# Kernel optimization log

Hardware: AMD Instinct MI355X
Metric: run time of the kernel (lower is better)

## Reference

```python
import jax, jax.numpy as jnp
import numpy as np

B, SQ, SKV, D = 16, 2048, 2048, 256

def setup_inputs() -> dict:
    key = jax.random.key(0)
    k1, k2, k3 = jax.random.split(key, 3)
    x = jax.random.normal(k1, (B, SQ, D), dtype=jnp.float32)
    y = jax.random.normal(k2, (B, SKV, D), dtype=jnp.float32)
    attn_mask = jax.random.normal(k3, (B, SQ, SKV), dtype=jnp.float32)
    dropout = 0  # p=0 -> deterministic (F.dropout with p=0 is identity)
    return {"x": x, "y": y, "attn_mask": attn_mask, "dropout": dropout}

def reference(x, y, attn_mask, dropout):
    # qk = x @ y^T : [B, Sq, Skv]
    qk = jnp.einsum('bqd,bkd->bqk', x, y)
    # NOTE: original scales mask by 1/sqrt(y.size(-2)) = 1/sqrt(Skv), not sqrt(D)
    scale_factor = attn_mask / (y.shape[-2] ** 0.5)
    scaled_qk = qk * scale_factor  # multiplicative per-element mask
    softmax_qk = jax.nn.softmax(scaled_qk, axis=-1)
    # dropout p=0 -> identity (deterministic baseline)
    dropout_qk = softmax_qk
    output = jnp.einsum('bqk,bkd->bqd', dropout_qk, y)
    return output + x
```

## Files before the change

kernel.cpp:

```cpp
#include <hip/hip_runtime.h>
#include <stdint.h>

typedef unsigned short u16;
typedef unsigned int   u32;

#define NB   16
#define SQL  2048
#define SKVL 2048
#define DHD  256
#define BQ   64
#define BKV  32
#define NITER (SKVL / BKV)
#define KSS  264
#define VTG  328
#define PSS  40
#define SCALE 0.022097086912079612f

typedef __bf16 bf16x8 __attribute__((ext_vector_type(8)));
typedef float  f32x4  __attribute__((ext_vector_type(4)));

__device__ __forceinline__ u16 f2b(float f) {
    union { float f; u32 i; } v; v.f = f;
    u32 x = v.i;
    return (u16)((x + 0x7fffu + ((x >> 16) & 1u)) >> 16);
}

__global__ __launch_bounds__(256, 2)
void fa_kernel(const float* __restrict__ x, const float* __restrict__ y,
               const float* __restrict__ mask, float* __restrict__ out)
{
    __shared__ __align__(16) u16 Ks[BKV * KSS];
    __shared__ __align__(16) u32 Vt[16 * VTG];
    __shared__ __align__(16) u16 Ps[BQ * PSS];

    const int tid  = threadIdx.x;
    const int wv   = tid >> 6;
    const int lane = tid & 63;
    const int l16  = lane & 15;
    const int quad = lane >> 4;

    const int b  = blockIdx.x >> 5;
    const int q0 = (blockIdx.x & 31) * BQ;

    bf16x8 qfrag[8];
    {
        const float* xq = x + ((size_t)(b * SQL + q0 + wv * 16 + l16)) * DHD + quad * 8;
        #pragma unroll
        for (int s = 0; s < 8; ++s) {
            const float4 a = *(const float4*)(xq + s * 32);
            const float4 c = *(const float4*)(xq + s * 32 + 4);
            union { u32 w[4]; bf16x8 v; } u;
            u.w[0] = (u32)f2b(a.x) | ((u32)f2b(a.y) << 16);
            u.w[1] = (u32)f2b(a.z) | ((u32)f2b(a.w) << 16);
            u.w[2] = (u32)f2b(c.x) | ((u32)f2b(c.y) << 16);
            u.w[3] = (u32)f2b(c.z) | ((u32)f2b(c.w) << 16);
            qfrag[s] = u.v;
        }
    }

    f32x4 o[16] = {};
    float lsum[4] = {0.f, 0.f, 0.f, 0.f};

    const int kv2 = tid & 15;
    const int dc  = tid >> 4;
    const float* ybase = y + ((size_t)b * SKVL) * DHD;

    float4 r0[4], r1[4];
    {
        const float* p0 = ybase + (size_t)(2 * kv2) * DHD + dc * 16;
        const float* p1 = p0 + DHD;
        #pragma unroll
        for (int p = 0; p < 4; ++p) { r0[p] = *(const float4*)(p0 + p * 4);
                                      r1[p] = *(const float4*)(p1 + p * 4); }
    }

    const float* mbase = mask + ((size_t)(b * SQL + q0 + wv * 16 + quad * 4)) * SKVL;

    float mkc0[4], mkc1[4], mkn0[4], mkn1[4];
    #pragma unroll
    for (int r = 0; r < 4; ++r) {
        const float* mp = mbase + (size_t)r * SKVL;
        mkc0[r] = mp[l16];
        mkc1[r] = mp[16 + l16];
    }

    for (int it = 0; it < NITER; ++it) {
        const int kv0 = it * BKV;

        __syncthreads();
        {
            u16 e0[16], e1[16];
            #pragma unroll
            for (int p = 0; p < 4; ++p) {
                e0[p*4+0]=f2b(r0[p].x); e0[p*4+1]=f2b(r0[p].y);
                e0[p*4+2]=f2b(r0[p].z); e0[p*4+3]=f2b(r0[p].w);
                e1[p*4+0]=f2b(r1[p].x); e1[p*4+1]=f2b(r1[p].y);
                e1[p*4+2]=f2b(r1[p].z); e1[p*4+3]=f2b(r1[p].w);
            }
            union { u32 w[4]; uint4 q; } k0a, k0b, k1a, k1b;
            #pragma unroll
            for (int i = 0; i < 4; ++i) {
                k0a.w[i] = (u32)e0[2*i]     | ((u32)e0[2*i+1]   << 16);
                k0b.w[i] = (u32)e0[8+2*i]   | ((u32)e0[8+2*i+1] << 16);
                k1a.w[i] = (u32)e1[2*i]     | ((u32)e1[2*i+1]   << 16);
                k1b.w[i] = (u32)e1[8+2*i]   | ((u32)e1[8+2*i+1] << 16);
            }
            *(uint4*)(&Ks[(2*kv2)  *KSS + dc*16])     = k0a.q;
            *(uint4*)(&Ks[(2*kv2)  *KSS + dc*16 + 8]) = k0b.q;
            *(uint4*)(&Ks[(2*kv2+1)*KSS + dc*16])     = k1a.q;
            *(uint4*)(&Ks[(2*kv2+1)*KSS + dc*16 + 8]) = k1b.q;
            #pragma unroll
            for (int e = 0; e < 16; ++e)
                Vt[dc*VTG + e*20 + kv2] = (u32)e0[e] | ((u32)e1[e] << 16);
        }
        __syncthreads();

        if (it + 1 < NITER) {
            const float* p0 = ybase + (size_t)(kv0 + BKV + 2 * kv2) * DHD + dc * 16;
            const float* p1 = p0 + DHD;
            #pragma unroll
            for (int p = 0; p < 4; ++p) { r0[p] = *(const float4*)(p0 + p * 4);
                                          r1[p] = *(const float4*)(p1 + p * 4); }
        }

        {
            const int kvn = (it + 1 < NITER) ? (kv0 + BKV) : 0;
            #pragma unroll
            for (int r = 0; r < 4; ++r) {
                const float* mp = mbase + (size_t)r * SKVL + kvn;
                mkn0[r] = mp[l16];
                mkn1[r] = mp[16 + l16];
            }
        }

        f32x4 acc0 = {}, acc1 = {};
        #pragma unroll
        for (int s = 0; s < 8; ++s) {
            bf16x8 b0 = *(const bf16x8*)(&Ks[ l16      * KSS + s*32 + quad*8]);
            bf16x8 b1 = *(const bf16x8*)(&Ks[(16+l16)  * KSS + s*32 + quad*8]);
            acc0 = __builtin_amdgcn_mfma_f32_16x16x32_bf16(qfrag[s], b0, acc0, 0, 0, 0);
            acc1 = __builtin_amdgcn_mfma_f32_16x16x32_bf16(qfrag[s], b1, acc1, 0, 0, 0);
        }

        #pragma unroll
        for (int r = 0; r < 4; ++r) {
            float p0 = __expf(acc0[r] * mkc0[r] * SCALE);
            float p1 = __expf(acc1[r] * mkc1[r] * SCALE);
            lsum[r] += p0 + p1;
            u16* pr = &Ps[(wv*16 + quad*4 + r) * PSS];
            pr[l16]      = f2b(p0);
            pr[16 + l16] = f2b(p1);
        }

        bf16x8 afrag = *(const bf16x8*)(&Ps[(wv*16 + l16) * PSS + quad*8]);
        #pragma unroll
        for (int t = 0; t < 16; ++t) {
            bf16x8 bfrag = *(const bf16x8*)(&Vt[t*VTG + l16*20 + quad*4]);
            o[t] = __builtin_amdgcn_mfma_f32_16x16x32_bf16(afrag, bfrag, o[t], 0, 0, 0);
        }

        #pragma unroll
        for (int r = 0; r < 4; ++r) { mkc0[r] = mkn0[r]; mkc1[r] = mkn1[r]; }
    }

    #pragma unroll
    for (int r = 0; r < 4; ++r) {
        float v = lsum[r];
        v += __shfl_xor(v, 1);
        v += __shfl_xor(v, 2);
        v += __shfl_xor(v, 4);
        v += __shfl_xor(v, 8);
        lsum[r] = 1.0f / v;
    }

    const int qrow = q0 + wv * 16 + quad * 4;
    #pragma unroll
    for (int r = 0; r < 4; ++r) {
        const size_t rowoff = ((size_t)(b * SQL + qrow + r)) * DHD;
        #pragma unroll
        for (int t = 0; t < 16; ++t) {
            const int d = t * 16 + l16;
            out[rowoff + d] = o[t][r] * lsum[r] + x[rowoff + d];
        }
    }
}

extern "C" void kernel_launch(void* const* d_in, const int* in_sizes, int n_in,
                              void* d_out, int out_size, void* d_ws, size_t ws_size,
                              hipStream_t stream) {
    const float* x    = (const float*)d_in[0];
    const float* y    = (const float*)d_in[1];
    const float* mask = (const float*)d_in[2];
    float* out        = (float*)d_out;
    dim3 grid(NB * (SQL / BQ));
    fa_kernel<<<grid, 256, 0, stream>>>(x, y, mask, out);
}
```

Measured before the change: 501.7 us.

## Precompute bf16 K and transposed V in workspace, stream via async LDS loads

Adds a prepass kernel that converts y to bf16 once, in both a row-major swizzled layout for K and a transposed swizzled layout for V, and stores them in the workspace. The main kernel then uses direct global-to-LDS async copies of these tiles with 64-wide KV blocks and 32x32x16 MFMAs. Waves are split across query and KV halves, and row sums are reduced through shared memory. This removes the per-block fp32-to-bf16 conversion and scattered transposition of y, in exchange for an extra kernel launch, workspace traffic and more barriers per iteration. A fallback keeps the old kernel when the workspace is too small.

```diff
diff --git a/kernel.cpp b/kernel.cpp
--- a/kernel.cpp
+++ b/kernel.cpp
@@ -8,16 +8,11 @@
 #define SQL  2048
 #define SKVL 2048
 #define DHD  256
-#define BQ   64
-#define BKV  32
-#define NITER (SKVL / BKV)
-#define KSS  264
-#define VTG  328
-#define PSS  40
 #define SCALE 0.022097086912079612f
 
 typedef __bf16 bf16x8 __attribute__((ext_vector_type(8)));
 typedef float  f32x4  __attribute__((ext_vector_type(4)));
+typedef float  f32x16 __attribute__((ext_vector_type(16)));
 
 __device__ __forceinline__ u16 f2b(float f) {
     union { float f; u32 i; } v; v.f = f;
@@ -25,22 +20,243 @@
     return (u16)((x + 0x7fffu + ((x >> 16) & 1u)) >> 16);
 }
 
+__device__ __forceinline__ void async_cp16(const void* g, void* l) {
+    __builtin_amdgcn_global_load_lds(
+        (const __attribute__((address_space(1))) u32*)g,
+        (__attribute__((address_space(3))) u32*)l, 16, 0, 0);
+}
+
+__global__ __launch_bounds__(256)
+void prepass(const float* __restrict__ y, u16* __restrict__ ws)
+{
+    u16* yb  = ws;
+    u16* ybT = ws + 8388608;
+
+    const int tid = threadIdx.x;
+    if (blockIdx.x < 512) {
+        const int b   = blockIdx.x >> 5;
+        const int seg = blockIdx.x & 31;
+        const int r   = tid >> 2;
+        const int dq  = tid & 3;
+        const int kvg = seg * 64 + r;
+        const float* src = y + ((size_t)(b * SKVL + kvg)) * DHD + dq * 64;
+        u16* dst = yb + ((size_t)(b * SKVL + kvg)) * DHD;
+        #pragma unroll
+        for (int j = 0; j < 8; ++j) {
+            const float4 a = *(const float4*)(src + j * 8);
+            const float4 c4 = *(const float4*)(src + j * 8 + 4);
+            union { u32 w[4]; uint4 q; } u;
+            u.w[0] = (u32)f2b(a.x)  | ((u32)f2b(a.y)  << 16);
+            u.w[1] = (u32)f2b(a.z)  | ((u32)f2b(a.w)  << 16);
+            u.w[2] = (u32)f2b(c4.x) | ((u32)f2b(c4.y) << 16);
+            u.w[3] = (u32)f2b(c4.z) | ((u32)f2b(c4.w) << 16);
+            const int pos = (dq * 8 + j) ^ (kvg & 7);
+            *(uint4*)(dst + pos * 8) = u.q;
+        }
+    } else {
+        const int j     = blockIdx.x - 512;
+        const int b     = j >> 5;
+        const int kvblk = j & 31;
+        const int d     = tid;
+        const int kv0   = kvblk * 64;
+        u16* dst = ybT + ((size_t)(b * 32 + kvblk)) * 16384 + d * 64;
+        #pragma unroll
+        for (int c = 0; c < 8; ++c) {
+            float v[8];
+            #pragma unroll
+            for (int e = 0; e < 8; ++e)
+                v[e] = y[((size_t)(b * SKVL + kv0 + 8 * c + e)) * DHD + d];
+            union { u32 w[4]; uint4 q; } u;
+            #pragma unroll
+            for (int i = 0; i < 4; ++i)
+                u.w[i] = (u32)f2b(v[2 * i]) | ((u32)f2b(v[2 * i + 1]) << 16);
+            const int p = c ^ (d & 7);
+            *(uint4*)(dst + p * 8) = u.q;
+        }
+    }
+}
+
 __global__ __launch_bounds__(256, 2)
-void fa_kernel(const float* __restrict__ x, const float* __restrict__ y,
-               const float* __restrict__ mask, float* __restrict__ out)
+void fa_main(const float* __restrict__ x, const float* __restrict__ mask,
+             const u16* __restrict__ ws, float* __restrict__ out)
 {
-    __shared__ __align__(16) u16 Ks[BKV * KSS];
-    __shared__ __align__(16) u32 Vt[16 * VTG];
-    __shared__ __align__(16) u16 Ps[BQ * PSS];
+    __shared__ __align__(16) u16 Ks[16384];
+    __shared__ __align__(16) u16 Vt[16384];
+    __shared__ __align__(16) u16 Ps[64 * 72];
+    __shared__ float Lred[2][64];
+
+    const u16* yb  = ws;
+    const u16* ybT = ws + 8388608;
+
+    const int tid  = threadIdx.x;
+    const int wv   = tid >> 6;
+    const int lane = tid & 63;
+    const int n    = lane & 31;
+    const int hi   = lane >> 5;
+    const int qh   = wv & 1;
+    const int kh   = wv >> 1;
+
+    const int b  = blockIdx.x >> 5;
+    const int q0 = (blockIdx.x & 31) * 64;
+
+    bf16x8 qfrag[16];
+    {
+        const float* xq = x + ((size_t)(b * SQL + q0 + 32 * qh + n)) * DHD + 8 * hi;
+        #pragma unroll
+        for (int s = 0; s < 16; ++s) {
+            const float4 a  = *(const float4*)(xq + s * 16);
+            const float4 c4 = *(const float4*)(xq + s * 16 + 4);
+            union { u32 w[4]; bf16x8 v; } u;
+            u.w[0] = (u32)f2b(a.x)  | ((u32)f2b(a.y)  << 16);
+            u.w[1] = (u32)f2b(a.z)  | ((u32)f2b(a.w)  << 16);
+            u.w[2] = (u32)f2b(c4.x) | ((u32)f2b(c4.y) << 16);
+            u.w[3] = (u32)f2b(c4.z) | ((u32)f2b(c4.w) << 16);
+            qfrag[s] = u.v;
+        }
+    }
+
+    f32x16 o0 = {}, o1 = {}, o2 = {}, o3 = {};
+    float lsum[16];
+    #pragma unroll
+    for (int r = 0; r < 16; ++r) lsum[r] = 0.f;
+
+    const float* mrow = mask + ((size_t)(b * SQL + q0 + 32 * qh + 4 * hi)) * SKVL
+                             + 32 * kh + n;
+    #define ROFF(r) ((size_t)(((r) & 3) + 8 * ((r) >> 2)) * SKVL)
+
+    float mkc[16], mkn[16];
+    #pragma unroll
+    for (int r = 0; r < 16; ++r) mkc[r] = mrow[ROFF(r)];
+
+    {
+        const char* gk = (const char*)(yb + ((size_t)b * SKVL) * DHD) + wv * 8192 + lane * 16;
+        const char* gv = (const char*)(ybT + ((size_t)b * 32) * 16384) + wv * 8192 + lane * 16;
+        char* lk = ((char*)Ks) + wv * 8192;
+        char* lv = ((char*)Vt) + wv * 8192;
+        #pragma unroll
+        for (int i = 0; i < 8; ++i) { async_cp16(gk + i * 1024, lk + i * 1024);
+                                      async_cp16(gv + i * 1024, lv + i * 1024); }
+    }
+    __syncthreads();
+
+    for (int it = 0; it < 32; ++it) {
+        const size_t kvn = (it + 1 < 32) ? (size_t)(it + 1) * 64 : 0;
+        #pragma unroll
+        for (int r = 0; r < 16; ++r) mkn[r] = mrow[ROFF(r) + kvn];
+
+        f32x16 sacc = {};
+        const int kvloc = 32 * kh + n;
+        #pragma unroll
+        for (int s = 0; s < 16; ++s) {
+            const int p = (2 * s + hi) ^ (kvloc & 7);
+            bf16x8 bf = *(const bf16x8*)(&Ks[kvloc * 256 + p * 8]);
+            sacc = __builtin_amdgcn_mfma_f32_32x32x16_bf16(qfrag[s], bf, sacc, 0, 0, 0);
+        }
+
+        #pragma unroll
+        for (int r = 0; r < 16; ++r) {
+            const int rowloc = (r & 3) + 8 * (r >> 2) + 4 * hi;
+            float pv = __expf(sacc[r] * mkc[r] * SCALE);
+            lsum[r] += pv;
+            Ps[(32 * qh + rowloc) * 72 + 32 * kh + n] = f2b(pv);
+        }
+
+        __syncthreads();
+
+        if (it + 1 < 32) {
+            const char* gk = (const char*)(yb + ((size_t)(b * SKVL + (it + 1) * 64)) * DHD)
+                             + wv * 8192 + lane * 16;
+            char* lk = ((char*)Ks) + wv * 8192;
+            #pragma unroll
+            for (int i = 0; i < 8; ++i) async_cp16(gk + i * 1024, lk + i * 1024);
+        }
+
+        bf16x8 pa[4];
+        #pragma unroll
+        for (int s = 0; s < 4; ++s)
+            pa[s] = *(const bf16x8*)(&Ps[(32 * qh + n) * 72 + 16 * s + 8 * hi]);
+        #pragma unroll
+        for (int t = 0; t < 4; ++t) {
+            const int d = 128 * kh + 32 * t + n;
+            f32x16 acc = (t == 0) ? o0 : (t == 1) ? o1 : (t == 2) ? o2 : o3;
+            #pragma unroll
+            for (int s = 0; s < 4; ++s) {
+                const int p = (2 * s + hi) ^ (d & 7);
+                bf16x8 bf = *(const bf16x8*)(&Vt[d * 64 + p * 8]);
+                acc = __builtin_amdgcn_mfma_f32_32x32x16_bf16(pa[s], bf, acc, 0, 0, 0);
+            }
+            if (t == 0) o0 = acc; else if (t == 1) o1 = acc; else if (t == 2) o2 = acc; else o3 = acc;
+        }
+
+        __syncthreads();
+
+        if (it + 1 < 32) {
+            const char* gv = (const char*)(ybT + ((size_t)(b * 32 + it + 1)) * 16384)
+                             + wv * 8192 + lane * 16;
+            char* lv = ((char*)Vt) + wv * 8192;
+            #pragma unroll
+            for (int i = 0; i < 8; ++i) async_cp16(gv + i * 1024, lv + i * 1024);
+        }
+        __syncthreads();
+
+        #pragma unroll
+        for (int r = 0; r < 16; ++r) mkc[r] = mkn[r];
+    }
+
+    #pragma unroll
+    for (int r = 0; r < 16; ++r) {
+        float v = lsum[r];
+        v += __shfl_xor(v, 1);
+        v += __shfl_xor(v, 2);
+        v += __shfl_xor(v, 4);
+        v += __shfl_xor(v, 8);
+        v += __shfl_xor(v, 16);
+        if (n == 0) {
+            const int rowloc = (r & 3) + 8 * (r >> 2) + 4 * hi;
+            Lred[kh][32 * qh + rowloc] = v;
+        }
+    }
+    __syncthreads();
+
+    float inv[16];
+    #pragma unroll
+    for (int r = 0; r < 16; ++r) {
+        const int qloc = 32 * qh + (r & 3) + 8 * (r >> 2) + 4 * hi;
+        inv[r] = 1.0f / (Lred[0][qloc] + Lred[1][qloc]);
+    }
+
+    #pragma unroll
+    for (int r = 0; r < 16; ++r) {
+        const int qloc = 32 * qh + (r & 3) + 8 * (r >> 2) + 4 * hi;
+        const size_t rowoff = ((size_t)(b * SQL + q0 + qloc)) * DHD;
+        #pragma unroll
+        for (int t = 0; t < 4; ++t) {
+            const int d = 128 * kh + 32 * t + n;
+            const float ov = (t == 0) ? o0[r] : (t == 1) ? o1[r] : (t == 2) ? o2[r] : o3[r];
+            out[rowoff + d] = ov * inv[r] + x[rowoff + d];
+        }
+    }
+}
+
+#define FKSS 264
+#define FVTG 328
+#define FPSS 40
+
+__global__ __launch_bounds__(256, 2)
+void fa_fallback(const float* __restrict__ x, const float* __restrict__ y,
+                 const float* __restrict__ mask, float* __restrict__ out)
+{
+    __shared__ __align__(16) u16 Ks[32 * FKSS];
+    __shared__ __align__(16) u32 Vt[16 * FVTG];
+    __shared__ __align__(16) u16 Ps[64 * FPSS];
 
     const int tid  = threadIdx.x;
     const int wv   = tid >> 6;
     const int lane = tid & 63;
     const int l16  = lane & 15;
     const int quad = lane >> 4;
-
     const int b  = blockIdx.x >> 5;
-    const int q0 = (blockIdx.x & 31) * BQ;
+    const int q0 = (blockIdx.x & 31) * 64;
 
     bf16x8 qfrag[8];
     {
@@ -57,14 +273,11 @@
             qfrag[s] = u.v;
         }
     }
-
     f32x4 o[16] = {};
-    float lsum[4] = {0.f, 0.f, 0.f, 0.f};
-
+    float ls[4] = {0.f, 0.f, 0.f, 0.f};
     const int kv2 = tid & 15;
     const int dc  = tid >> 4;
     const float* ybase = y + ((size_t)b * SKVL) * DHD;
-
     float4 r0[4], r1[4];
     {
         const float* p0 = ybase + (size_t)(2 * kv2) * DHD + dc * 16;
@@ -73,20 +286,15 @@
         for (int p = 0; p < 4; ++p) { r0[p] = *(const float4*)(p0 + p * 4);
                                       r1[p] = *(const float4*)(p1 + p * 4); }
     }
-
     const float* mbase = mask + ((size_t)(b * SQL + q0 + wv * 16 + quad * 4)) * SKVL;
-
     float mkc0[4], mkc1[4], mkn0[4], mkn1[4];
     #pragma unroll
     for (int r = 0; r < 4; ++r) {
         const float* mp = mbase + (size_t)r * SKVL;
-        mkc0[r] = mp[l16];
-        mkc1[r] = mp[16 + l16];
-    }
-
-    for (int it = 0; it < NITER; ++it) {
-        const int kv0 = it * BKV;
-
+        mkc0[r] = mp[l16]; mkc1[r] = mp[16 + l16];
+    }
+    for (int it = 0; it < 64; ++it) {
+        const int kv0 = it * 32;
         __syncthreads();
         {
             u16 e0[16], e1[16];
@@ -100,79 +308,68 @@
             union { u32 w[4]; uint4 q; } k0a, k0b, k1a, k1b;
             #pragma unroll
             for (int i = 0; i < 4; ++i) {
-                k0a.w[i] = (u32)e0[2*i]     | ((u32)e0[2*i+1]   << 16);
-                k0b.w[i] = (u32)e0[8+2*i]   | ((u32)e0[8+2*i+1] << 16);
-                k1a.w[i] = (u32)e1[2*i]     | ((u32)e1[2*i+1]   << 16);
-                k1b.w[i] = (u32)e1[8+2*i]   | ((u32)e1[8+2*i+1] << 16);
+                k0a.w[i] = (u32)e0[2*i]   | ((u32)e0[2*i+1]   << 16);
+                k0b.w[i] = (u32)e0[8+2*i] | ((u32)e0[8+2*i+1] << 16);
+                k1a.w[i] = (u32)e1[2*i]   | ((u32)e1[2*i+1]   << 16);
+                k1b.w[i] = (u32)e1[8+2*i] | ((u32)e1[8+2*i+1] << 16);
             }
-            *(uint4*)(&Ks[(2*kv2)  *KSS + dc*16])     = k0a.q;
-            *(uint4*)(&Ks[(2*kv2)  *KSS + dc*16 + 8]) = k0b.q;
-            *(uint4*)(&Ks[(2*kv2+1)*KSS + dc*16])     = k1a.q;
-            *(uint4*)(&Ks[(2*kv2+1)*KSS + dc*16 + 8]) = k1b.q;
+            *(uint4*)(&Ks[(2*kv2)  *FKSS + dc*16])     = k0a.q;
+            *(uint4*)(&Ks[(2*kv2)  *FKSS + dc*16 + 8]) = k0b.q;
+            *(uint4*)(&Ks[(2*kv2+1)*FKSS + dc*16])     = k1a.q;
+            *(uint4*)(&Ks[(2*kv2+1)*FKSS + dc*16 + 8]) = k1b.q;
             #pragma unroll
             for (int e = 0; e < 16; ++e)
-                Vt[dc*VTG + e*20 + kv2] = (u32)e0[e] | ((u32)e1[e] << 16);
-        }
-        __syncthreads();
-
-        if (it + 1 < NITER) {
-            const float* p0 = ybase + (size_t)(kv0 + BKV + 2 * kv2) * DHD + dc * 16;
+                Vt[dc*FVTG + e*20 + kv2] = (u32)e0[e] | ((u32)e1[e] << 16);
+        }
+        __syncthreads();
+        if (it + 1 < 64) {
+            const float* p0 = ybase + (size_t)(kv0 + 32 + 2 * kv2) * DHD + dc * 16;
             const float* p1 = p0 + DHD;
             #pragma unroll
             for (int p = 0; p < 4; ++p) { r0[p] = *(const float4*)(p0 + p * 4);
                                           r1[p] = *(const float4*)(p1 + p * 4); }
         }
-
         {
-            const int kvn = (it + 1 < NITER) ? (kv0 + BKV) : 0;
+            const int kvn2 = (it + 1 < 64) ? (kv0 + 32) : 0;
             #pragma unroll
             for (int r = 0; r < 4; ++r) {
-                const float* mp = mbase + (size_t)r * SKVL + kvn;
-                mkn0[r] = mp[l16];
-                mkn1[r] = mp[16 + l16];
+                const float* mp = mbase + (size_t)r * SKVL + kvn2;
+                mkn0[r] = mp[l16]; mkn1[r] = mp[16 + l16];
             }
         }
-
         f32x4 acc0 = {}, acc1 = {};
         #pragma unroll
         for (int s = 0; s < 8; ++s) {
-            bf16x8 b0 = *(const bf16x8*)(&Ks[ l16      * KSS + s*32 + quad*8]);
-            bf16x8 b1 = *(const bf16x8*)(&Ks[(16+l16)  * KSS + s*32 + quad*8]);
+            bf16x8 b0 = *(const bf16x8*)(&Ks[ l16     * FKSS + s*32 + quad*8]);
+            bf16x8 b1 = *(const bf16x8*)(&Ks[(16+l16) * FKSS + s*32 + quad*8]);
             acc0 = __builtin_amdgcn_mfma_f32_16x16x32_bf16(qfrag[s], b0, acc0, 0, 0, 0);
             acc1 = __builtin_amdgcn_mfma_f32_16x16x32_bf16(qfrag[s], b1, acc1, 0, 0, 0);
         }
-
         #pragma unroll
         for (int r = 0; r < 4; ++r) {
             float p0 = __expf(acc0[r] * mkc0[r] * SCALE);
             float p1 = __expf(acc1[r] * mkc1[r] * SCALE);
-            lsum[r] += p0 + p1;
-            u16* pr = &Ps[(wv*16 + quad*4 + r) * PSS];
+            ls[r] += p0 + p1;
+            u16* pr = &Ps[(wv*16 + quad*4 + r) * FPSS];
             pr[l16]      = f2b(p0);
             pr[16 + l16] = f2b(p1);
         }
-
-        bf16x8 afrag = *(const bf16x8*)(&Ps[(wv*16 + l16) * PSS + quad*8]);
+        bf16x8 afrag = *(const bf16x8*)(&Ps[(wv*16 + l16) * FPSS + quad*8]);
         #pragma unroll
         for (int t = 0; t < 16; ++t) {
-            bf16x8 bfrag = *(const bf16x8*)(&Vt[t*VTG + l16*20 + quad*4]);
+            bf16x8 bfrag = *(const bf16x8*)(&Vt[t*FVTG + l16*20 + quad*4]);
             o[t] = __builtin_amdgcn_mfma_f32_16x16x32_bf16(afrag, bfrag, o[t], 0, 0, 0);
         }
-
         #pragma unroll
         for (int r = 0; r < 4; ++r) { mkc0[r] = mkn0[r]; mkc1[r] = mkn1[r]; }
     }
-
     #pragma unroll
     for (int r = 0; r < 4; ++r) {
-        float v = lsum[r];
-        v += __shfl_xor(v, 1);
-        v += __shfl_xor(v, 2);
-        v += __shfl_xor(v, 4);
-        v += __shfl_xor(v, 8);
-        lsum[r] = 1.0f / v;
-    }
-
+        float v = ls[r];
+        v += __shfl_xor(v, 1); v += __shfl_xor(v, 2);
+        v += __shfl_xor(v, 4); v += __shfl_xor(v, 8);
+        ls[r] = 1.0f / v;
+    }
     const int qrow = q0 + wv * 16 + quad * 4;
     #pragma unroll
     for (int r = 0; r < 4; ++r) {
@@ -180,7 +377,7 @@
         #pragma unroll
         for (int t = 0; t < 16; ++t) {
             const int d = t * 16 + l16;
-            out[rowoff + d] = o[t][r] * lsum[r] + x[rowoff + d];
+            out[rowoff + d] = o[t][r] * ls[r] + x[rowoff + d];
         }
     }
 }
@@ -192,6 +389,11 @@
     const float* y    = (const float*)d_in[1];
     const float* mask = (const float*)d_in[2];
     float* out        = (float*)d_out;
-    dim3 grid(NB * (SQL / BQ));
-    fa_kernel<<<grid, 256, 0, stream>>>(x, y, mask, out);
-}
+
+    if (ws_size >= 33554432ull) {
+        prepass<<<1024, 256, 0, stream>>>(y, (u16*)d_ws);
+        fa_main<<<512, 256, 0, stream>>>(x, mask, (const u16*)d_ws, out);
+    } else {
+        fa_fallback<<<512, 256, 0, stream>>>(x, y, mask, out);
+    }
+}
```

New measurement: 472.7 us. 1.06x faster.
